# Performance work log

Measured on AMD Instinct MI355X. Metric: run time of the kernel, lower is better.

The kernel has to match this reference:

```python
import jax, jax.numpy as jnp
import numpy as np

N_NODES = 8192
N_EDGES = 262144
N_REL = 8
NUM_CLASSES = 151
EMB = 256
BOX = 1024
HID = 512
OUT = 256
N_TASKS = 2


def setup_inputs() -> dict:
    key = jax.random.key(0)
    ks = jax.random.split(key, 20)
    w = lambda k, shape: jax.random.normal(k, shape, dtype=jnp.float32) * 0.02
    return {
        "box_features": jax.random.normal(ks[0], (N_NODES, BOX), dtype=jnp.float32),
        "pred_labels": jax.random.randint(ks[1], (N_NODES,), 0, NUM_CLASSES),
        "edge_index": jax.random.randint(ks[2], (2, N_EDGES), 0, N_NODES),
        "edge_type": jax.random.randint(ks[3], (N_EDGES,), 0, N_REL),
        "nodes_per_graph": 128,
        "emb_table": w(ks[4], (NUM_CLASSES, EMB)),
        "W_lin": w(ks[5], (BOX + EMB, HID)),
        "b_lin": jnp.zeros((HID,), jnp.float32),
        "rel_W1": w(ks[6], (N_REL, HID, HID)),
        "root_W1": w(ks[7], (HID, HID)),
        "b1": jnp.zeros((HID,), jnp.float32),
        "rel_W2": w(ks[8], (N_REL, HID, OUT)),
        "root_W2": w(ks[9], (HID, OUT)),
        "b2": jnp.zeros((OUT,), jnp.float32),
        "Wc1": w(ks[10], (OUT, OUT)),
        "bc1": jnp.zeros((OUT,), jnp.float32),
        "Wc2": w(ks[11], (OUT, N_TASKS)),
        "bc2": jnp.zeros((N_TASKS,), jnp.float32),
    }


def rgcn_conv(x, src, dst, etype, rel_W, root_W, b):
    """PyG RGCNConv: per-relation mean aggregation + root weight + bias."""
    R, _, out_dim = rel_W.shape
    N = x.shape[0]
    transformed = jnp.einsum('ni,rio->rno', x, rel_W)      # [R, N, out]
    msg = transformed[etype, src]                           # [E, out] gather per edge
    seg = etype * N + dst                                   # (relation, dst) segment id
    sums = jax.ops.segment_sum(msg, seg, num_segments=R * N)
    cnt = jax.ops.segment_sum(jnp.ones((msg.shape[0],), x.dtype), seg, num_segments=R * N)
    mean = sums / jnp.maximum(cnt, 1.0)[:, None]
    agg = mean.reshape(R, N, out_dim).sum(0)                # sum over relations
    return agg + x @ root_W + b


def reference(box_features, pred_labels, edge_index, edge_type, nodes_per_graph,
              emb_table, W_lin, b_lin, rel_W1, root_W1, b1, rel_W2, root_W2, b2,
              Wc1, bc1, Wc2, bc2):
    src, dst = edge_index[0], edge_index[1]
    # obj embedding + concat with box features
    x = jnp.concatenate([box_features, emb_table[pred_labels]], axis=-1)  # [N, 1280]
    x = x @ W_lin + b_lin                                                  # [N, 512]
    x = jax.nn.relu(rgcn_conv(x, src, dst, edge_type, rel_W1, root_W1, b1))
    x = rgcn_conv(x, src, dst, edge_type, rel_W2, root_W2, b2)             # [N, 256]
    # mean graph pooling over equal-size graphs
    B = x.shape[0] // nodes_per_graph
    pooled = x.reshape(B, nodes_per_graph, -1).mean(axis=1)                # [B, 256]
    # classifier (dropout is identity in eval)
    y_logits = (pooled @ Wc1 + bc1) @ Wc2 + bc2                            # [B, n_tasks]
    y_prob = jax.nn.softmax(y_logits, axis=-1)
    return y_logits, y_prob
```

## Files before the change

kernel.cpp:

```cpp
#include <hip/hip_runtime.h>
#include <cstdint>

#define NNODES 8192
#define NEDGES 262144
#define NRELS  8
#define EMBD   256
#define BOXD   1024
#define HIDD   512
#define OUTD   256
#define NSEG   (NRELS * NNODES)
#define K0DIM  (BOXD + EMBD)
#define KSDIM  (NRELS * HIDD + HIDD)

using bf16x8 = __attribute__((ext_vector_type(8))) short;
using f32x4  = __attribute__((ext_vector_type(4))) float;
using us4    = __attribute__((ext_vector_type(4))) unsigned short;

__device__ __forceinline__ unsigned short f2b(float f) {
    union { float f; uint32_t u; } v; v.f = f;
    uint32_t r = v.u + 0x7FFFu + ((v.u >> 16) & 1u);
    return (unsigned short)(r >> 16);
}

__device__ __forceinline__ us4 cvt4(f32x4 v) {
    us4 u;
    u[0] = f2b(v[0]); u[1] = f2b(v[1]); u[2] = f2b(v[2]); u[3] = f2b(v[3]);
    return u;
}

__device__ __forceinline__ float b2f_lo(uint32_t w) {
    union { uint32_t u; float f; } v; v.u = w << 16; return v.f;
}
__device__ __forceinline__ float b2f_hi(uint32_t w) {
    union { uint32_t u; float f; } v; v.u = w & 0xffff0000u; return v.f;
}

__global__ void k_build_x0(const float* __restrict__ box, const int* __restrict__ labels,
                           const float* __restrict__ emb, unsigned short* __restrict__ X0) {
    int n = blockIdx.x;
    int lab = labels[n];
    const f32x4* b = (const f32x4*)(box + (size_t)n * BOXD);
    const f32x4* e = (const f32x4*)(emb + (size_t)lab * EMBD);
    us4* o = (us4*)(X0 + (size_t)n * K0DIM);
    for (int j = threadIdx.x; j < K0DIM / 4; j += 256) {
        f32x4 v = (j < BOXD / 4) ? b[j] : e[j - BOXD / 4];
        o[j] = cvt4(v);
    }
}

__global__ void k_transpose_all(const float* __restrict__ W_lin, const float* __restrict__ rel_W1,
                                const float* __restrict__ root_W1, const float* __restrict__ rel_W2,
                                const float* __restrict__ root_W2,
                                unsigned short* __restrict__ W0t, unsigned short* __restrict__ W1t,
                                unsigned short* __restrict__ W2t) {
    __shared__ float t[32][33];
    int bid = blockIdx.x;
    const float* src; unsigned short* dst; int No, ld, kOff, kb, ob;
    if (bid < 640)        { int g = bid;        src = W_lin;   dst = W0t; No = 512; ld = K0DIM; kOff = 0;    kb = g % 40;  ob = g / 40; }
    else if (bid < 2688)  { int g = bid - 640;  src = rel_W1;  dst = W1t; No = 512; ld = KSDIM; kOff = 0;    kb = g % 128; ob = g / 128; }
    else if (bid < 2944)  { int g = bid - 2688; src = root_W1; dst = W1t; No = 512; ld = KSDIM; kOff = 4096; kb = g % 16;  ob = g / 16; }
    else if (bid < 3968)  { int g = bid - 2944; src = rel_W2;  dst = W2t; No = 256; ld = KSDIM; kOff = 0;    kb = g % 128; ob = g / 128; }
    else                  { int g = bid - 3968; src = root_W2; dst = W2t; No = 256; ld = KSDIM; kOff = 4096; kb = g % 16;  ob = g / 16; }
    int kt = kb * 32, ot = ob * 32;
    int tx = threadIdx.x & 31, ty = threadIdx.x >> 5;
#pragma unroll
    for (int i = 0; i < 4; i++) {
        int k = kt + ty + i * 8;
        t[ty + i * 8][tx] = src[(size_t)k * No + ot + tx];
    }
    __syncthreads();
#pragma unroll
    for (int i = 0; i < 4; i++) {
        int o = ot + ty + i * 8;
        dst[(size_t)o * ld + kOff + kt + tx] = f2b(t[tx][ty + i * 8]);
    }
}

__global__ void k_hist(const int* __restrict__ etype, const int* __restrict__ edst,
                       int* __restrict__ cnt) {
    int e = blockIdx.x * 256 + threadIdx.x;
    if (e >= NEDGES) return;
    atomicAdd(&cnt[etype[e] * NNODES + edst[e]], 1);
}

__global__ __launch_bounds__(1024) void k_scan(const int* __restrict__ cnt,
                                               int* __restrict__ segstart) {
    __shared__ int part[1024];
    __shared__ int sup[16];
    __shared__ int supx[16];
    int t = threadIdx.x;
    int base = t * 64;
    int s = 0;
    for (int i = 0; i < 64; i++) s += cnt[base + i];
    part[t] = s;
    __syncthreads();
    if (t < 16) {
        int a = 0;
        for (int i = 0; i < 64; i++) a += part[t * 64 + i];
        sup[t] = a;
    }
    __syncthreads();
    if (t == 0) {
        int a = 0;
        for (int i = 0; i < 16; i++) { supx[i] = a; a += sup[i]; }
    }
    __syncthreads();
    int a = supx[t >> 6];
    for (int i = (t & ~63); i < t; i++) a += part[i];
    for (int i = 0; i < 64; i++) { segstart[base + i] = a; a += cnt[base + i]; }
    if (t == 1023) segstart[NSEG] = a;
}

__global__ void k_scatter(const int* __restrict__ etype, const int* __restrict__ esrc,
                          const int* __restrict__ edst, const int* __restrict__ segstart,
                          int* __restrict__ cursor, int* __restrict__ esorted) {
    int e = blockIdx.x * 256 + threadIdx.x;
    if (e >= NEDGES) return;
    int key = etype[e] * NNODES + edst[e];
    int pos = atomicAdd(&cursor[key], 1);
    esorted[segstart[key] + pos] = esrc[e];
}

__global__ __launch_bounds__(256) void k_aggregate(
        const unsigned short* __restrict__ x, const int* __restrict__ segstart,
        const int* __restrict__ esorted, unsigned short* __restrict__ Xin) {
    int seg = blockIdx.x * 4 + (threadIdx.x >> 6);
    int lane = threadIdx.x & 63;
    int r = seg >> 13;
    int dstn = seg & (NNODES - 1);
    float a[8] = {0, 0, 0, 0, 0, 0, 0, 0};
    float b[8] = {0, 0, 0, 0, 0, 0, 0, 0};
    int s0 = segstart[seg], s1 = segstart[seg + 1];
    int t = s0;
    for (; t + 2 <= s1; t += 2) {
        uint4 v0 = *(const uint4*)(x + (size_t)esorted[t] * HIDD + lane * 8);
        uint4 v1 = *(const uint4*)(x + (size_t)esorted[t + 1] * HIDD + lane * 8);
        a[0] += b2f_lo(v0.x); a[1] += b2f_hi(v0.x);
        a[2] += b2f_lo(v0.y); a[3] += b2f_hi(v0.y);
        a[4] += b2f_lo(v0.z); a[5] += b2f_hi(v0.z);
        a[6] += b2f_lo(v0.w); a[7] += b2f_hi(v0.w);
        b[0] += b2f_lo(v1.x); b[1] += b2f_hi(v1.x);
        b[2] += b2f_lo(v1.y); b[3] += b2f_hi(v1.y);
        b[4] += b2f_lo(v1.z); b[5] += b2f_hi(v1.z);
        b[6] += b2f_lo(v1.w); b[7] += b2f_hi(v1.w);
    }
    if (t < s1) {
        uint4 v0 = *(const uint4*)(x + (size_t)esorted[t] * HIDD + lane * 8);
        a[0] += b2f_lo(v0.x); a[1] += b2f_hi(v0.x);
        a[2] += b2f_lo(v0.y); a[3] += b2f_hi(v0.y);
        a[4] += b2f_lo(v0.z); a[5] += b2f_hi(v0.z);
        a[6] += b2f_lo(v0.w); a[7] += b2f_hi(v0.w);
    }
    float iv = (s1 > s0) ? (1.0f / (float)(s1 - s0)) : 1.0f;
#pragma unroll
    for (int j = 0; j < 8; j++) a[j] = (a[j] + b[j]) * iv;
    uint4 u;
    u.x = (uint32_t)f2b(a[0]) | ((uint32_t)f2b(a[1]) << 16);
    u.y = (uint32_t)f2b(a[2]) | ((uint32_t)f2b(a[3]) << 16);
    u.z = (uint32_t)f2b(a[4]) | ((uint32_t)f2b(a[5]) << 16);
    u.w = (uint32_t)f2b(a[6]) | ((uint32_t)f2b(a[7]) << 16);
    *(uint4*)(Xin + (size_t)dstn * KSDIM + r * HIDD + lane * 8) = u;
}

__global__ __launch_bounds__(256, 2) void k_gemm(
        const unsigned short* __restrict__ A,
        const unsigned short* __restrict__ Bt,
        float* __restrict__ P,
        int M, int N, int K, int Kc) {
    __shared__ unsigned short As[2][128 * 64];
    __shared__ unsigned short Bs[2][128 * 64];
    const int tid = threadIdx.x;
    const int lane = tid & 63, wid = tid >> 6;
    const int tiles_m = M >> 7;
    const int tm = blockIdx.x % tiles_m, tn = blockIdx.x / tiles_m;
    const int m0 = tm << 7, n0 = tn << 7;
    const int wr = wid >> 1, wc = wid & 1;
    const int k0 = blockIdx.y * Kc;

    f32x4 acc[4][4];
#pragma unroll
    for (int i = 0; i < 4; i++)
#pragma unroll
        for (int j = 0; j < 4; j++) acc[i][j] = (f32x4){0.f, 0.f, 0.f, 0.f};

    const int rowg = tid >> 3;
    const int srcc = (tid & 7) ^ (rowg & 7);
    const unsigned short* gA = A  + (size_t)(m0 + rowg) * K + k0 + srcc * 8;
    const unsigned short* gB = Bt + (size_t)(n0 + rowg) * K + k0 + srcc * 8;
    const int ldsbase = wid * 512;

    auto stage = [&](int bsel, int kt) {
#pragma unroll
        for (int i = 0; i < 4; ++i) {
            __builtin_amdgcn_global_load_lds(
                (const __attribute__((address_space(1))) void*)(gA + kt + i * 32 * K),
                (__attribute__((address_space(3))) void*)&As[bsel][i * 2048 + ldsbase], 16, 0, 0);
            __builtin_amdgcn_global_load_lds(
                (const __attribute__((address_space(1))) void*)(gB + kt + i * 32 * K),
                (__attribute__((address_space(3))) void*)&Bs[bsel][i * 2048 + ldsbase], 16, 0, 0);
        }
    };

    const int arow = wr * 64 + (lane & 15);
    const int brow = wc * 64 + (lane & 15);
    const int l7 = lane & 7;
    const int c0 = lane >> 4;

    const int nt = Kc >> 6;
    int cur = 0;
    stage(0, 0);
    asm volatile("s_waitcnt vmcnt(0)" ::: "memory");
    __builtin_amdgcn_s_barrier();

    for (int t = 0; t < nt; ++t) {
        if (t + 1 < nt) stage(cur ^ 1, (t + 1) * 64);
#pragma unroll
        for (int s4 = 0; s4 < 2; ++s4) {
            const int slot = (c0 + s4 * 4) ^ l7;
            bf16x8 af[4], bfr[4];
#pragma unroll
            for (int m = 0; m < 4; m++)
                af[m] = *(const bf16x8*)&As[cur][(arow + m * 16) * 64 + slot * 8];
#pragma unroll
            for (int n = 0; n < 4; n++)
                bfr[n] = *(const bf16x8*)&Bs[cur][(brow + n * 16) * 64 + slot * 8];
#pragma unroll
            for (int m = 0; m < 4; m++)
#pragma unroll
                for (int n = 0; n < 4; n++)
                    acc[m][n] = __builtin_amdgcn_mfma_f32_16x16x32_bf16(af[m], bfr[n], acc[m][n], 0, 0, 0);
        }
        if (t + 1 < nt) {
            asm volatile("s_waitcnt vmcnt(0)" ::: "memory");
            __builtin_amdgcn_s_barrier();
            cur ^= 1;
        }
    }

    float* Pout = P + (size_t)blockIdx.y * M * N;
    const int crow0 = m0 + wr * 64 + (lane >> 4) * 4;
    const int ccol0 = n0 + wc * 64 + (lane & 15);
#pragma unroll
    for (int n = 0; n < 4; n++) {
        int col = ccol0 + n * 16;
#pragma unroll
        for (int m = 0; m < 4; m++)
#pragma unroll
            for (int r = 0; r < 4; r++)
                Pout[(size_t)(crow0 + m * 16 + r) * N + col] = acc[m][n][r];
    }
}

template <int RELU>
__global__ void k_reduce_bf(const float* __restrict__ P, const float* __restrict__ bias,
                            unsigned short* __restrict__ xbf, unsigned short* __restrict__ Xin,
                            int MN) {
    int idx = (blockIdx.x * 256 + threadIdx.x) * 4;
    f32x4 v = *(const f32x4*)&P[idx];
    v += *(const f32x4*)&P[(size_t)MN + idx];
    v += *(const f32x4*)&bias[idx & 511];
    if (RELU) {
#pragma unroll
        for (int j = 0; j < 4; j++) v[j] = fmaxf(v[j], 0.f);
    }
    us4 u = cvt4(v);
    *(us4*)&xbf[idx] = u;
    int row = idx >> 9, col = idx & 511;
    *(us4*)&Xin[(size_t)row * KSDIM + NRELS * HIDD + col] = u;
}

__global__ void k_reduce4(const float* P, const float* __restrict__ bias,
                          float* out, int MN, int N) {
    int idx = (blockIdx.x * 256 + threadIdx.x) * 4;
    f32x4 v = *(const f32x4*)&P[idx];
#pragma unroll
    for (int s = 1; s < 4; s++) v += *(const f32x4*)&P[(size_t)s * MN + idx];
    v += *(const f32x4*)&bias[idx & (N - 1)];
    *(f32x4*)&out[idx] = v;
}

__global__ void k_poolclass(const float* __restrict__ x3, const float* __restrict__ Wc1,
                            const float* __restrict__ bc1, const float* __restrict__ Wc2,
                            const float* __restrict__ bc2, float* __restrict__ out) {
    __shared__ float p[256];
    __shared__ float h[256];
    __shared__ float lg[2];
    int b = blockIdx.x, o = threadIdx.x;
    float s = 0.f;
    for (int i = 0; i < 128; i++) s += x3[(size_t)(b * 128 + i) * OUTD + o];
    p[o] = s * (1.0f / 128.0f);
    __syncthreads();
    float s1 = bc1[o];
    for (int i = 0; i < 256; i++) s1 += p[i] * Wc1[i * 256 + o];
    h[o] = s1;
    __syncthreads();
    if (o < 2) {
        float t = bc2[o];
        for (int i = 0; i < 256; i++) t += h[i] * Wc2[i * 2 + o];
        lg[o] = t;
        out[b * 2 + o] = t;
    }
    __syncthreads();
    if (o == 0) {
        float m = fmaxf(lg[0], lg[1]);
        float e0 = expf(lg[0] - m), e1 = expf(lg[1] - m);
        float inv = 1.0f / (e0 + e1);
        out[128 + b * 2 + 0] = e0 * inv;
        out[128 + b * 2 + 1] = e1 * inv;
    }
}

extern "C" void kernel_launch(void* const* d_in, const int* in_sizes, int n_in,
                              void* d_out, int out_size, void* d_ws, size_t ws_size,
                              hipStream_t stream) {
    const float* box     = (const float*)d_in[0];
    const int*   labels  = (const int*)d_in[1];
    const int*   eidx    = (const int*)d_in[2];
    const int*   etype   = (const int*)d_in[3];
    const float* emb     = (const float*)d_in[5];
    const float* W_lin   = (const float*)d_in[6];
    const float* b_lin   = (const float*)d_in[7];
    const float* rel_W1  = (const float*)d_in[8];
    const float* root_W1 = (const float*)d_in[9];
    const float* b1      = (const float*)d_in[10];
    const float* rel_W2  = (const float*)d_in[11];
    const float* root_W2 = (const float*)d_in[12];
    const float* b2      = (const float*)d_in[13];
    const float* Wc1     = (const float*)d_in[14];
    const float* bc1     = (const float*)d_in[15];
    const float* Wc2     = (const float*)d_in[16];
    const float* bc2     = (const float*)d_in[17];
    const int* esrc = eidx;
    const int* edst = eidx + NEDGES;

    char* ws = (char*)d_ws;
    size_t off = 0;
    auto alloc = [&](size_t bytes) -> char* {
        char* p = ws + off;
        off += (bytes + 255) & ~(size_t)255;
        return p;
    };
    float* Pp = (float*)alloc((size_t)2 * NNODES * HIDD * 4);
    float* x3 = Pp;
    unsigned short* X0   = (unsigned short*)alloc((size_t)NNODES * K0DIM * 2);
    unsigned short* xbf  = X0;
    unsigned short* W0t  = (unsigned short*)alloc((size_t)HIDD * K0DIM * 2);
    unsigned short* W1t  = (unsigned short*)alloc((size_t)HIDD * KSDIM * 2);
    unsigned short* W2t  = (unsigned short*)alloc((size_t)OUTD * KSDIM * 2);
    unsigned short* Xin  = (unsigned short*)alloc((size_t)NNODES * KSDIM * 2);
    int*   cnt     = (int*)alloc((size_t)NSEG * 4);
    int*   cursor  = (int*)alloc((size_t)NSEG * 4);
    int*   segst   = (int*)alloc((size_t)(NSEG + 1) * 4);
    int*   esorted = (int*)alloc((size_t)NEDGES * 4);
    if (off > ws_size) return;

    float* out = (float*)d_out;

    hipMemsetAsync(cnt, 0, (size_t)2 * NSEG * 4, stream);
    k_build_x0<<<NNODES, 256, 0, stream>>>(box, labels, emb, X0);
    k_transpose_all<<<4096, 256, 0, stream>>>(W_lin, rel_W1, root_W1, rel_W2, root_W2,
                                              W0t, W1t, W2t);
    k_hist<<<NEDGES / 256, 256, 0, stream>>>(etype, edst, cnt);
    k_scan<<<1, 1024, 0, stream>>>(cnt, segst);
    k_scatter<<<NEDGES / 256, 256, 0, stream>>>(etype, esrc, edst, segst, cursor, esorted);

    k_gemm<<<dim3((NNODES / 128) * (HIDD / 128), 2), 256, 0, stream>>>(
        X0, W0t, Pp, NNODES, HIDD, K0DIM, K0DIM / 2);
    k_reduce_bf<0><<<(NNODES * HIDD) / 1024, 256, 0, stream>>>(
        Pp, b_lin, xbf, Xin, NNODES * HIDD);

    k_aggregate<<<NSEG / 4, 256, 0, stream>>>(xbf, segst, esorted, Xin);
    k_gemm<<<dim3((NNODES / 128) * (HIDD / 128), 2), 256, 0, stream>>>(
        Xin, W1t, Pp, NNODES, HIDD, KSDIM, KSDIM / 2);
    k_reduce_bf<1><<<(NNODES * HIDD) / 1024, 256, 0, stream>>>(
        Pp, b1, xbf, Xin, NNODES * HIDD);

    k_aggregate<<<NSEG / 4, 256, 0, stream>>>(xbf, segst, esorted, Xin);
    k_gemm<<<dim3((NNODES / 128) * (OUTD / 128), 4), 256, 0, stream>>>(
        Xin, W2t, Pp, NNODES, OUTD, KSDIM, KSDIM / 4);
    k_reduce4<<<(NNODES * OUTD) / 1024, 256, 0, stream>>>(
        Pp, b2, x3, NNODES * OUTD, OUTD);

    k_poolclass<<<64, 256, 0, stream>>>(x3, Wc1, bc1, Wc2, bc2, out);
}
```

Baseline: 282.0 us.

## Pool before second RGCN layer GEMM and enlarge GEMM tiles to 256x256

Because the second RGCN layer is linear and is followed only by mean pooling, the layer is reordered so that per-relation means and the root input are first pooled per graph. A small GEMV head (k_head1) then replaces the full 8192-row layer-2 GEMM, its reduction and its aggregate pass. Separately, the main GEMM moves to 256x256 tiles with 512 threads and a K-step of 32. Split-K is raised to 4 when the workspace is large enough. This trades a different floating-point summation order and higher register pressure for removing most of the layer-2 work.

```diff
diff --git a/kernel.cpp b/kernel.cpp
--- a/kernel.cpp
+++ b/kernel.cpp
@@ -162,74 +162,114 @@
     *(uint4*)(Xin + (size_t)dstn * KSDIM + r * HIDD + lane * 8) = u;
 }
 
-__global__ __launch_bounds__(256, 2) void k_gemm(
+__global__ __launch_bounds__(256) void k_aggpool(
+        const unsigned short* __restrict__ x, const int* __restrict__ segstart,
+        const int* __restrict__ esorted, float* __restrict__ PXin) {
+    int g = blockIdx.x >> 3, r = blockIdx.x & 7;
+    int wave = threadIdx.x >> 6, lane = threadIdx.x & 63;
+    float a[8] = {0, 0, 0, 0, 0, 0, 0, 0};
+    for (int d8 = wave; d8 < 128; d8 += 4) {
+        int seg = r * NNODES + g * 128 + d8;
+        int s0 = segstart[seg], s1 = segstart[seg + 1];
+        if (s0 == s1) continue;
+        float p[8] = {0, 0, 0, 0, 0, 0, 0, 0};
+        for (int t = s0; t < s1; ++t) {
+            uint4 v = *(const uint4*)(x + (size_t)esorted[t] * HIDD + lane * 8);
+            p[0] += b2f_lo(v.x); p[1] += b2f_hi(v.x);
+            p[2] += b2f_lo(v.y); p[3] += b2f_hi(v.y);
+            p[4] += b2f_lo(v.z); p[5] += b2f_hi(v.z);
+            p[6] += b2f_lo(v.w); p[7] += b2f_hi(v.w);
+        }
+        float w = 1.0f / (128.0f * (float)(s1 - s0));
+#pragma unroll
+        for (int j = 0; j < 8; j++) a[j] += p[j] * w;
+    }
+    __shared__ float red[4][512];
+#pragma unroll
+    for (int j = 0; j < 8; j++) red[wave][lane * 8 + j] = a[j];
+    __syncthreads();
+    for (int c = threadIdx.x; c < 512; c += 256) {
+        float s = red[0][c] + red[1][c] + red[2][c] + red[3][c];
+        PXin[(size_t)g * KSDIM + r * 512 + c] = s;
+    }
+}
+
+__global__ void k_rootpool(const unsigned short* __restrict__ x, float* __restrict__ PXin) {
+    int g = blockIdx.x;
+    for (int c = threadIdx.x; c < 512; c += 256) {
+        float s = 0.f;
+        for (int n = 0; n < 128; n++) {
+            unsigned short w = x[(size_t)(g * 128 + n) * HIDD + c];
+            union { uint32_t u; float f; } v; v.u = (uint32_t)w << 16;
+            s += v.f;
+        }
+        PXin[(size_t)g * KSDIM + 4096 + c] = s * (1.0f / 128.0f);
+    }
+}
+
+__global__ __launch_bounds__(512, 2) void k_gemm(
         const unsigned short* __restrict__ A,
         const unsigned short* __restrict__ Bt,
         float* __restrict__ P,
         int M, int N, int K, int Kc) {
-    __shared__ unsigned short As[2][128 * 64];
-    __shared__ unsigned short Bs[2][128 * 64];
+    __shared__ unsigned short As[2][8192];
+    __shared__ unsigned short Bs[2][8192];
     const int tid = threadIdx.x;
     const int lane = tid & 63, wid = tid >> 6;
-    const int tiles_m = M >> 7;
+    const int tiles_m = M >> 8;
     const int tm = blockIdx.x % tiles_m, tn = blockIdx.x / tiles_m;
-    const int m0 = tm << 7, n0 = tn << 7;
-    const int wr = wid >> 1, wc = wid & 1;
+    const int m0 = tm << 8, n0 = tn << 8;
+    const int wr = wid >> 2, wc = wid & 3;
     const int k0 = blockIdx.y * Kc;
 
-    f32x4 acc[4][4];
-#pragma unroll
-    for (int i = 0; i < 4; i++)
+    f32x4 acc[8][4];
+#pragma unroll
+    for (int i = 0; i < 8; i++)
 #pragma unroll
         for (int j = 0; j < 4; j++) acc[i][j] = (f32x4){0.f, 0.f, 0.f, 0.f};
 
-    const int rowg = tid >> 3;
-    const int srcc = (tid & 7) ^ (rowg & 7);
+    const int rowg = tid >> 2;
+    const int srcc = (tid & 3) ^ ((tid >> 4) & 3);
     const unsigned short* gA = A  + (size_t)(m0 + rowg) * K + k0 + srcc * 8;
     const unsigned short* gB = Bt + (size_t)(n0 + rowg) * K + k0 + srcc * 8;
     const int ldsbase = wid * 512;
 
     auto stage = [&](int bsel, int kt) {
 #pragma unroll
-        for (int i = 0; i < 4; ++i) {
+        for (int i = 0; i < 2; ++i) {
             __builtin_amdgcn_global_load_lds(
-                (const __attribute__((address_space(1))) void*)(gA + kt + i * 32 * K),
-                (__attribute__((address_space(3))) void*)&As[bsel][i * 2048 + ldsbase], 16, 0, 0);
+                (const __attribute__((address_space(1))) void*)(gA + kt + (size_t)i * 128 * K),
+                (__attribute__((address_space(3))) void*)&As[bsel][i * 4096 + ldsbase], 16, 0, 0);
             __builtin_amdgcn_global_load_lds(
-                (const __attribute__((address_space(1))) void*)(gB + kt + i * 32 * K),
-                (__attribute__((address_space(3))) void*)&Bs[bsel][i * 2048 + ldsbase], 16, 0, 0);
+                (const __attribute__((address_space(1))) void*)(gB + kt + (size_t)i * 128 * K),
+                (__attribute__((address_space(3))) void*)&Bs[bsel][i * 4096 + ldsbase], 16, 0, 0);
         }
     };
 
-    const int arow = wr * 64 + (lane & 15);
+    const int arow = wr * 128 + (lane & 15);
     const int brow = wc * 64 + (lane & 15);
-    const int l7 = lane & 7;
-    const int c0 = lane >> 4;
-
-    const int nt = Kc >> 6;
+    const int slot = (lane >> 4) ^ ((lane >> 2) & 3);
+
+    const int nt = Kc >> 5;
     int cur = 0;
     stage(0, 0);
     asm volatile("s_waitcnt vmcnt(0)" ::: "memory");
     __builtin_amdgcn_s_barrier();
 
     for (int t = 0; t < nt; ++t) {
-        if (t + 1 < nt) stage(cur ^ 1, (t + 1) * 64);
-#pragma unroll
-        for (int s4 = 0; s4 < 2; ++s4) {
-            const int slot = (c0 + s4 * 4) ^ l7;
-            bf16x8 af[4], bfr[4];
-#pragma unroll
-            for (int m = 0; m < 4; m++)
-                af[m] = *(const bf16x8*)&As[cur][(arow + m * 16) * 64 + slot * 8];
+        if (t + 1 < nt) stage(cur ^ 1, (t + 1) * 32);
+        bf16x8 af[8], bfr[4];
+#pragma unroll
+        for (int m = 0; m < 8; m++)
+            af[m] = *(const bf16x8*)&As[cur][(arow + m * 16) * 32 + slot * 8];
+#pragma unroll
+        for (int n = 0; n < 4; n++)
+            bfr[n] = *(const bf16x8*)&Bs[cur][(brow + n * 16) * 32 + slot * 8];
+#pragma unroll
+        for (int m = 0; m < 8; m++)
 #pragma unroll
             for (int n = 0; n < 4; n++)
-                bfr[n] = *(const bf16x8*)&Bs[cur][(brow + n * 16) * 64 + slot * 8];
-#pragma unroll
-            for (int m = 0; m < 4; m++)
-#pragma unroll
-                for (int n = 0; n < 4; n++)
-                    acc[m][n] = __builtin_amdgcn_mfma_f32_16x16x32_bf16(af[m], bfr[n], acc[m][n], 0, 0, 0);
-        }
+                acc[m][n] = __builtin_amdgcn_mfma_f32_16x16x32_bf16(af[m], bfr[n], acc[m][n], 0, 0, 0);
         if (t + 1 < nt) {
             asm volatile("s_waitcnt vmcnt(0)" ::: "memory");
             __builtin_amdgcn_s_barrier();
@@ -238,26 +278,26 @@
     }
 
     float* Pout = P + (size_t)blockIdx.y * M * N;
-    const int crow0 = m0 + wr * 64 + (lane >> 4) * 4;
+    const int crow0 = m0 + wr * 128 + (lane >> 4) * 4;
     const int ccol0 = n0 + wc * 64 + (lane & 15);
 #pragma unroll
     for (int n = 0; n < 4; n++) {
         int col = ccol0 + n * 16;
 #pragma unroll
-        for (int m = 0; m < 4; m++)
+        for (int m = 0; m < 8; m++)
 #pragma unroll
             for (int r = 0; r < 4; r++)
                 Pout[(size_t)(crow0 + m * 16 + r) * N + col] = acc[m][n][r];
     }
 }
 
-template <int RELU>
+template <int RELU, int WROOT>
 __global__ void k_reduce_bf(const float* __restrict__ P, const float* __restrict__ bias,
                             unsigned short* __restrict__ xbf, unsigned short* __restrict__ Xin,
-                            int MN) {
+                            int MN, int S) {
     int idx = (blockIdx.x * 256 + threadIdx.x) * 4;
     f32x4 v = *(const f32x4*)&P[idx];
-    v += *(const f32x4*)&P[(size_t)MN + idx];
+    for (int s = 1; s < S; s++) v += *(const f32x4*)&P[(size_t)s * MN + idx];
     v += *(const f32x4*)&bias[idx & 511];
     if (RELU) {
 #pragma unroll
@@ -265,30 +305,45 @@
     }
     us4 u = cvt4(v);
     *(us4*)&xbf[idx] = u;
-    int row = idx >> 9, col = idx & 511;
-    *(us4*)&Xin[(size_t)row * KSDIM + NRELS * HIDD + col] = u;
-}
-
-__global__ void k_reduce4(const float* P, const float* __restrict__ bias,
-                          float* out, int MN, int N) {
-    int idx = (blockIdx.x * 256 + threadIdx.x) * 4;
-    f32x4 v = *(const f32x4*)&P[idx];
-#pragma unroll
-    for (int s = 1; s < 4; s++) v += *(const f32x4*)&P[(size_t)s * MN + idx];
-    v += *(const f32x4*)&bias[idx & (N - 1)];
-    *(f32x4*)&out[idx] = v;
-}
-
-__global__ void k_poolclass(const float* __restrict__ x3, const float* __restrict__ Wc1,
-                            const float* __restrict__ bc1, const float* __restrict__ Wc2,
-                            const float* __restrict__ bc2, float* __restrict__ out) {
+    if (WROOT) {
+        int row = idx >> 9, col = idx & 511;
+        *(us4*)&Xin[(size_t)row * KSDIM + NRELS * HIDD + col] = u;
+    }
+}
+
+__global__ void k_head1(const float* __restrict__ PXin, const unsigned short* __restrict__ W2t,
+                        const float* __restrict__ b2, float* __restrict__ pooled) {
+    __shared__ float red[4][64];
+    int g = blockIdx.x >> 2;
+    int ob = (blockIdx.x & 3) * 64;
+    int ol = threadIdx.x & 63, kq = threadIdx.x >> 6;
+    const float* p = PXin + (size_t)g * KSDIM + kq * 1152;
+    const unsigned short* w = W2t + (size_t)(ob + ol) * KSDIM + kq * 1152;
+    float s = 0.f;
+    for (int k = 0; k < 1152; k += 8) {
+        uint4 wv = *(const uint4*)(w + k);
+        s += p[k + 0] * b2f_lo(wv.x) + p[k + 1] * b2f_hi(wv.x)
+           + p[k + 2] * b2f_lo(wv.y) + p[k + 3] * b2f_hi(wv.y)
+           + p[k + 4] * b2f_lo(wv.z) + p[k + 5] * b2f_hi(wv.z)
+           + p[k + 6] * b2f_lo(wv.w) + p[k + 7] * b2f_hi(wv.w);
+    }
+    red[kq][ol] = s;
+    __syncthreads();
+    if (threadIdx.x < 64) {
+        float t = red[0][threadIdx.x] + red[1][threadIdx.x]
+                + red[2][threadIdx.x] + red[3][threadIdx.x];
+        pooled[g * 256 + ob + threadIdx.x] = t + b2[ob + threadIdx.x];
+    }
+}
+
+__global__ void k_head2(const float* __restrict__ pooled, const float* __restrict__ Wc1,
+                        const float* __restrict__ bc1, const float* __restrict__ Wc2,
+                        const float* __restrict__ bc2, float* __restrict__ out) {
     __shared__ float p[256];
     __shared__ float h[256];
     __shared__ float lg[2];
     int b = blockIdx.x, o = threadIdx.x;
-    float s = 0.f;
-    for (int i = 0; i < 128; i++) s += x3[(size_t)(b * 128 + i) * OUTD + o];
-    p[o] = s * (1.0f / 128.0f);
+    p[o] = pooled[b * 256 + o];
     __syncthreads();
     float s1 = bc1[o];
     for (int i = 0; i < 256; i++) s1 += p[i] * Wc1[i * 256 + o];
@@ -334,20 +389,30 @@
     const int* edst = eidx + NEDGES;
 
     char* ws = (char*)d_ws;
+    size_t fixed = (size_t)NNODES * KSDIM * 2
+                 + (size_t)NNODES * HIDD * 2
+                 + (size_t)HIDD * K0DIM * 2 + (size_t)HIDD * KSDIM * 2
+                 + (size_t)OUTD * KSDIM * 2
+                 + (size_t)64 * KSDIM * 4 + 64 * OUTD * 4
+                 + (size_t)(3 * NSEG + 1) * 4 + (size_t)NEDGES * 4
+                 + 16 * 256;
+    int S = (ws_size >= fixed + (size_t)4 * NNODES * HIDD * 4) ? 4 : 2;
+
     size_t off = 0;
     auto alloc = [&](size_t bytes) -> char* {
         char* p = ws + off;
         off += (bytes + 255) & ~(size_t)255;
         return p;
     };
-    float* Pp = (float*)alloc((size_t)2 * NNODES * HIDD * 4);
-    float* x3 = Pp;
-    unsigned short* X0   = (unsigned short*)alloc((size_t)NNODES * K0DIM * 2);
-    unsigned short* xbf  = X0;
-    unsigned short* W0t  = (unsigned short*)alloc((size_t)HIDD * K0DIM * 2);
-    unsigned short* W1t  = (unsigned short*)alloc((size_t)HIDD * KSDIM * 2);
-    unsigned short* W2t  = (unsigned short*)alloc((size_t)OUTD * KSDIM * 2);
-    unsigned short* Xin  = (unsigned short*)alloc((size_t)NNODES * KSDIM * 2);
+    float* Pp = (float*)alloc((size_t)S * NNODES * HIDD * 4);
+    unsigned short* Xin = (unsigned short*)alloc((size_t)NNODES * KSDIM * 2);
+    unsigned short* X0  = Xin;
+    unsigned short* xbf = (unsigned short*)alloc((size_t)NNODES * HIDD * 2);
+    unsigned short* W0t = (unsigned short*)alloc((size_t)HIDD * K0DIM * 2);
+    unsigned short* W1t = (unsigned short*)alloc((size_t)HIDD * KSDIM * 2);
+    unsigned short* W2t = (unsigned short*)alloc((size_t)OUTD * KSDIM * 2);
+    float* PXin   = (float*)alloc((size_t)64 * KSDIM * 4);
+    float* pooled = (float*)alloc((size_t)64 * OUTD * 4);
     int*   cnt     = (int*)alloc((size_t)NSEG * 4);
     int*   cursor  = (int*)alloc((size_t)NSEG * 4);
     int*   segst   = (int*)alloc((size_t)(NSEG + 1) * 4);
@@ -355,6 +420,7 @@
     if (off > ws_size) return;
 
     float* out = (float*)d_out;
+    const int MN = NNODES * HIDD;
 
     hipMemsetAsync(cnt, 0, (size_t)2 * NSEG * 4, stream);
     k_build_x0<<<NNODES, 256, 0, stream>>>(box, labels, emb, X0);
@@ -364,22 +430,15 @@
     k_scan<<<1, 1024, 0, stream>>>(cnt, segst);
     k_scatter<<<NEDGES / 256, 256, 0, stream>>>(etype, esrc, edst, segst, cursor, esorted);
 
-    k_gemm<<<dim3((NNODES / 128) * (HIDD / 128), 2), 256, 0, stream>>>(
-        X0, W0t, Pp, NNODES, HIDD, K0DIM, K0DIM / 2);
-    k_reduce_bf<0><<<(NNODES * HIDD) / 1024, 256, 0, stream>>>(
-        Pp, b_lin, xbf, Xin, NNODES * HIDD);
+    k_gemm<<<dim3(64, S), 512, 0, stream>>>(X0, W0t, Pp, NNODES, HIDD, K0DIM, K0DIM / S);
+    k_reduce_bf<0, 1><<<MN / 1024, 256, 0, stream>>>(Pp, b_lin, xbf, Xin, MN, S);
 
     k_aggregate<<<NSEG / 4, 256, 0, stream>>>(xbf, segst, esorted, Xin);
-    k_gemm<<<dim3((NNODES / 128) * (HIDD / 128), 2), 256, 0, stream>>>(
-        Xin, W1t, Pp, NNODES, HIDD, KSDIM, KSDIM / 2);
-    k_reduce_bf<1><<<(NNODES * HIDD) / 1024, 256, 0, stream>>>(
-        Pp, b1, xbf, Xin, NNODES * HIDD);
-
-    k_aggregate<<<NSEG / 4, 256, 0, stream>>>(xbf, segst, esorted, Xin);
-    k_gemm<<<dim3((NNODES / 128) * (OUTD / 128), 4), 256, 0, stream>>>(
-        Xin, W2t, Pp, NNODES, OUTD, KSDIM, KSDIM / 4);
-    k_reduce4<<<(NNODES * OUTD) / 1024, 256, 0, stream>>>(
-        Pp, b2, x3, NNODES * OUTD, OUTD);
-
-    k_poolclass<<<64, 256, 0, stream>>>(x3, Wc1, bc1, Wc2, bc2, out);
-}
+    k_gemm<<<dim3(64, S), 512, 0, stream>>>(Xin, W1t, Pp, NNODES, HIDD, KSDIM, KSDIM / S);
+    k_reduce_bf<1, 0><<<MN / 1024, 256, 0, stream>>>(Pp, b1, xbf, Xin, MN, S);
+
+    k_aggpool<<<512, 256, 0, stream>>>(xbf, segst, esorted, PXin);
+    k_rootpool<<<64, 256, 0, stream>>>(xbf, PXin);
+    k_head1<<<256, 256, 0, stream>>>(PXin, W2t, b2, pooled);
+    k_head2<<<64, 256, 0, stream>>>(pooled, Wc1, bc1, Wc2, bc2, out);
+}
```

Measured after the change: 369.2 us. 30.9% more time.
